# Kernel optimization log

Hardware: AMD Instinct MI355X
Metric: run time of the kernel (lower is better)

## Reference

```python
import jax, jax.numpy as jnp
import numpy as np

N = 50_000      # num_nodes
E = 1_600_000   # num_edges
R = 8           # num_relations
D = 128         # hidden_dim
L = 3           # num_layers
EPS = 1e-5


def setup_inputs() -> dict:
    key = jax.random.key(0)
    ks = jax.random.split(key, 10)
    x = jnp.arange(N, dtype=jnp.int64) if jax.config.jax_enable_x64 else jnp.arange(N, dtype=jnp.int32)
    edge_index = jax.random.randint(ks[0], (2, E), 0, N)
    edge_type = jax.random.randint(ks[1], (E,), 0, R)
    emb = jax.random.normal(ks[2], (N, D), dtype=jnp.float32) * (1.0 / np.sqrt(D))
    w_rel = jax.random.normal(ks[3], (L, R, D, D), dtype=jnp.float32) * (1.0 / np.sqrt(D))
    w_root = jax.random.normal(ks[4], (L, D, D), dtype=jnp.float32) * (1.0 / np.sqrt(D))
    bias = jax.random.normal(ks[5], (L, D), dtype=jnp.float32) * 0.01
    gamma = 1.0 + 0.1 * jax.random.normal(ks[6], (L, D), dtype=jnp.float32)
    beta = 0.1 * jax.random.normal(ks[7], (L, D), dtype=jnp.float32)
    return {"x": x, "edge_index": edge_index, "edge_type": edge_type,
            "emb": emb, "w_rel": w_rel, "w_root": w_root, "bias": bias,
            "gamma": gamma, "beta": beta}


def _layer_norm(h, g, b):
    mu = jnp.mean(h, axis=-1, keepdims=True)
    var = jnp.mean(jnp.square(h - mu), axis=-1, keepdims=True)
    return (h - mu) * jax.lax.rsqrt(var + EPS) * g + b


def _rgcn_conv(h, src, dst, etype, w_rel, w_root, b):
    # PyG RGCNConv: per-relation mean aggregation of transformed neighbors + root transform + bias
    hr = jnp.einsum('nd,rdf->rnf', h, w_rel)          # [R, N, D] relation-transformed features
    msg = hr[etype, src]                               # [E, D] gather per edge
    seg = etype * N + dst                              # combined (relation, target) segment id
    sums = jax.ops.segment_sum(msg, seg, num_segments=R * N)            # [R*N, D]
    cnt = jax.ops.segment_sum(jnp.ones((msg.shape[0],), h.dtype), seg, num_segments=R * N)
    mean = sums / jnp.maximum(cnt, 1.0)[:, None]
    agg = mean.reshape(R, N, D).sum(axis=0)            # sum over relations
    return agg + h @ w_root + b


def reference(x, edge_index, edge_type, emb, w_rel, w_root, bias, gamma, beta):
    src, dst = edge_index[0], edge_index[1]
    h = emb[x]                                         # node embedding lookup
    for i in range(L):
        h_new = _rgcn_conv(h, src, dst, edge_type, w_rel[i], w_root[i], bias[i])
        h_new = jax.nn.relu(_layer_norm(h_new, gamma[i], beta[i]))
        # dropout is identity in eval/reference mode
        h = h + h_new if i > 0 else h_new
    return h
```

## Files before the change

kernel.cpp:

```cpp
#include <hip/hip_runtime.h>

#define NN 50000
#define NE 1600000
#define NR 8
#define ND 128
#define NL 3
#define RN (NR * NN)
#define LN_EPS 1e-5f
#define PADF 132

#define NBKT 196
#define BSH 11
#define STRIDE_PB 10240
#define BIN_BLOCKS 500
#define EPB 3200
#define I4PB 800
#define MM_BLOCKS ((NN + 63) / 64)

#define PREP_G (NN * 64)
#define PREP_W (27 * 16384)
#define PREP_TOT (PREP_G + PREP_W)
#define PREP_BLOCKS ((PREP_TOT + 255) / 256)

#define WS_H    0
#define WS_ROW  14400000
#define WS_BCUR 16000064
#define WS_ADJ  16004096
#define WS_WB   22404096
#define WS_BIG  23288832
#define WS_NEED_NEW (23288832ULL + 9ULL * NN * 256)

typedef __attribute__((ext_vector_type(8))) short short8;
typedef __attribute__((ext_vector_type(4))) float float4v;
typedef __attribute__((ext_vector_type(4))) unsigned uint4v;

__device__ __forceinline__ float bflo(unsigned u) { return __uint_as_float(u << 16); }
__device__ __forceinline__ float bfhi(unsigned u) { return __uint_as_float(u & 0xFFFF0000u); }
__device__ __forceinline__ unsigned f2bf(float f) {
    unsigned u = __float_as_uint(f);
    return (u + 0x7FFFu + ((u >> 16) & 1u)) >> 16;
}
__device__ __forceinline__ unsigned pack2(float lo, float hi) {
    return f2bf(lo) | (f2bf(hi) << 16);
}

__global__ __launch_bounds__(256) void k_prepbin(const int* __restrict__ x,
                                                 const float* __restrict__ emb,
                                                 const float* __restrict__ w_rel,
                                                 const float* __restrict__ w_root,
                                                 const int* __restrict__ src,
                                                 const int* __restrict__ dst,
                                                 const int* __restrict__ et,
                                                 unsigned* __restrict__ h,
                                                 unsigned short* __restrict__ wb,
                                                 int* __restrict__ bcur,
                                                 unsigned* __restrict__ stage) {
    __shared__ int lcnt[256];
    __shared__ int loff[256];
    __shared__ int lcur[256];
    __shared__ int sbase[256];
    __shared__ int tmp[256];
    __shared__ unsigned srt[EPB];
    __shared__ unsigned char bkt[EPB];

    int tid = threadIdx.x;
    if (blockIdx.x >= BIN_BLOCKS) {
        int i = (blockIdx.x - BIN_BLOCKS) * 256 + tid;
        if (i < PREP_G) {
            int n = i >> 6, dw = i & 63;
            float2 v = *(const float2*)&emb[(size_t)x[n] * ND + 2 * dw];
            h[i] = pack2(v.x, v.y);
            return;
        }
        i -= PREP_G;
        if (i < PREP_W) {
            int m = i >> 14;
            int idx = i & 16383;
            int j = idx & 7;
            int lane = (idx >> 3) & 63;
            int ft = (idx >> 9) & 7;
            int kk = idx >> 12;
            int row = kk * 32 + (lane >> 4) * 8 + j;
            int col = ft * 16 + (lane & 15);
            const float* W = (m < 24) ? (w_rel + (size_t)m * 16384)
                                      : (w_root + (size_t)(m - 24) * 16384);
            wb[i] = (unsigned short)f2bf(W[row * ND + col]);
        }
        return;
    }

    lcnt[tid] = 0;
    __syncthreads();

    int base4 = blockIdx.x * I4PB;
    const int4* s4p = (const int4*)src;
    const int4* d4p = (const int4*)dst;
    const int4* t4p = (const int4*)et;

    for (int i4 = tid; i4 < I4PB; i4 += 256) {
        int4 d4 = d4p[base4 + i4];
        int4 t4 = t4p[base4 + i4];
        atomicAdd(&lcnt[(t4.x * NN + d4.x) >> BSH], 1);
        atomicAdd(&lcnt[(t4.y * NN + d4.y) >> BSH], 1);
        atomicAdd(&lcnt[(t4.z * NN + d4.z) >> BSH], 1);
        atomicAdd(&lcnt[(t4.w * NN + d4.w) >> BSH], 1);
    }
    __syncthreads();
    int own = lcnt[tid];
    tmp[tid] = own;
    __syncthreads();
    for (int off = 1; off < 256; off <<= 1) {
        int v = (tid >= off) ? tmp[tid - off] : 0;
        __syncthreads();
        tmp[tid] += v;
        __syncthreads();
    }
    int excl = tmp[tid] - own;
    loff[tid] = excl;
    lcur[tid] = excl;
    if (tid < NBKT) sbase[tid] = atomicAdd(&bcur[tid], own);
    __syncthreads();

    for (int i4 = tid; i4 < I4PB; i4 += 256) {
        int4 s4 = s4p[base4 + i4];
        int4 d4 = d4p[base4 + i4];
        int4 t4 = t4p[base4 + i4];
        int segs[4] = {t4.x * NN + d4.x, t4.y * NN + d4.y,
                       t4.z * NN + d4.z, t4.w * NN + d4.w};
        int srcs[4] = {s4.x, s4.y, s4.z, s4.w};
#pragma unroll
        for (int j = 0; j < 4; j++) {
            int seg = segs[j];
            int b = seg >> BSH;
            unsigned rec = ((unsigned)(seg & 2047) << 16) | (unsigned)srcs[j];
            int pos = atomicAdd(&lcur[b], 1);
            srt[pos] = rec;
            bkt[pos] = (unsigned char)b;
        }
    }
    __syncthreads();
    for (int i = tid; i < EPB; i += 256) {
        int b = bkt[i];
        int idx = sbase[b] + (i - loff[b]);
        if (idx < STRIDE_PB)
            stage[(size_t)b * STRIDE_PB + idx] = srt[i];
    }
}

__device__ __forceinline__ void binB_body(const unsigned* __restrict__ stage,
                                          const int* __restrict__ bcur,
                                          int* __restrict__ rowstart,
                                          int* __restrict__ adj,
                                          int b, int tid,
                                          int* tmp, int* lcnt2, int* loff2,
                                          unsigned short* srt2, int* misc) {
    int bv = (tid < NBKT) ? bcur[tid] : 0;
    tmp[tid] = bv;
    __syncthreads();
    for (int off = 1; off < 256; off <<= 1) {
        int v = (tid >= off) ? tmp[tid - off] : 0;
        __syncthreads();
        tmp[tid] += v;
        __syncthreads();
    }
    if (tid == b) { misc[0] = tmp[tid] - bv; misc[1] = bv; }
    for (int j = tid; j < 2048; j += 256) lcnt2[j] = 0;
    __syncthreads();

    int n = misc[1];
    n = n < STRIDE_PB ? n : STRIDE_PB;
    const unsigned* sp = stage + (size_t)b * STRIDE_PB;
    for (int i = tid; i < n; i += 256)
        atomicAdd(&lcnt2[sp[i] >> 16], 1);
    __syncthreads();

    int v8[8];
    int s8 = 0;
    int base8 = tid * 8;
#pragma unroll
    for (int j = 0; j < 8; j++) { v8[j] = lcnt2[base8 + j]; s8 += v8[j]; }
    tmp[tid] = s8;
    __syncthreads();
    for (int off = 1; off < 256; off <<= 1) {
        int v = (tid >= off) ? tmp[tid - off] : 0;
        __syncthreads();
        tmp[tid] += v;
        __syncthreads();
    }
    int run = tmp[tid] - s8;
#pragma unroll
    for (int j = 0; j < 8; j++) { loff2[base8 + j] = run; run += v8[j]; }
    __syncthreads();
    for (int j = tid; j < 2048; j += 256) lcnt2[j] = loff2[j];
    __syncthreads();

    for (int i = tid; i < n; i += 256) {
        unsigned rec = sp[i];
        int pos = atomicAdd(&lcnt2[rec >> 16], 1);
        srt2[pos] = (unsigned short)(rec & 0xFFFFu);
    }
    __syncthreads();

    int gb = misc[0];
    for (int i = tid; i < n; i += 256) adj[gb + i] = (int)srt2[i];
    int segbase = b << BSH;
    for (int j = tid; j < 2048; j += 256) {
        int seg = segbase + j;
        if (seg < RN) rowstart[seg] = gb + loff2[j];
    }
    if (b == NBKT - 1 && tid == 0) rowstart[RN] = NE;
}

typedef unsigned TRarr[16][66];

__device__ __forceinline__ void mm_body(const unsigned* __restrict__ h32,
                                        const unsigned short* __restrict__ wrel,
                                        const unsigned short* __restrict__ wroot,
                                        unsigned* __restrict__ hr,
                                        int mb, int tid,
                                        uint4* SB4, TRarr* TRp) {
    const unsigned short* SBs = (const unsigned short*)SB4;
    int wave = tid >> 6, lane = tid & 63;
    int quad = lane >> 4, l15 = lane & 15;
    int w0w = mb * 64 + wave * 16;
    int gi = w0w + l15; gi = gi < NN ? gi : NN - 1;
    int pr = l15 & 1;

    const unsigned* Hrow = h32 + (size_t)gi * 64;
    short8 afr[4];
#pragma unroll
    for (int kk = 0; kk < 4; kk++)
        afr[kk] = *(const short8*)&Hrow[kk * 16 + quad * 4];

    for (int m = 0; m < 9; m++) {
        const unsigned short* W = (m < 8) ? (wrel + (size_t)m * 16384) : wroot;
        __syncthreads();
        {
            const uint4* Wg = (const uint4*)W;
#pragma unroll
            for (int i = 0; i < 8; i++) SB4[tid + 256 * i] = Wg[tid + 256 * i];
        }
        __syncthreads();

        float4v acc[8];
#pragma unroll
        for (int i = 0; i < 8; i++) acc[i] = (float4v){0.f, 0.f, 0.f, 0.f};
#pragma unroll
        for (int kk = 0; kk < 4; kk++) {
#pragma unroll
            for (int ft = 0; ft < 8; ft++) {
                short8 bf = *(const short8*)&SBs[((kk * 8 + ft) * 64 + lane) * 8];
                acc[ft] = __builtin_amdgcn_mfma_f32_16x16x32_bf16(afr[kk], bf, acc[ft], 0, 0, 0);
            }
        }

#pragma unroll
        for (int ft = 0; ft < 8; ft++) {
            float4v part;
#pragma unroll
            for (int rg = 0; rg < 4; rg++) part[rg] = __shfl_xor(acc[ft][rg], 1, 64);
            if ((ft & 1) == pr) {
                int a = l15 >> 1;
#pragma unroll
                for (int rg = 0; rg < 4; rg++) {
                    float lo = pr ? part[rg] : acc[ft][rg];
                    float hi = pr ? acc[ft][rg] : part[rg];
                    TRp[wave][quad * 4 + rg][ft * 8 + a] = pack2(lo, hi);
                }
            }
        }
        unsigned* hrm = hr + (size_t)m * NN * 64;
#pragma unroll
        for (int ps = 0; ps < 4; ps++) {
            int ri = ps * 4 + quad;
            uint4 v = *(const uint4*)&TRp[wave][ri][l15 * 4];
            int row = w0w + ri;
            if (row < NN)
                *(uint4*)&hrm[(size_t)row * 64 + l15 * 4] = v;
        }
    }
}

__global__ __launch_bounds__(256) void k_binB_mm(const unsigned* __restrict__ stage,
                                                 const int* __restrict__ bcur,
                                                 int* __restrict__ rowstart,
                                                 int* __restrict__ adj,
                                                 const unsigned* __restrict__ h32,
                                                 const unsigned short* __restrict__ wrel,
                                                 const unsigned short* __restrict__ wroot,
                                                 unsigned* __restrict__ hr) {
    __shared__ uint4 SMEM[3104];
    int tid = threadIdx.x;
    if (blockIdx.x < NBKT) {
        int* tmp = (int*)SMEM;
        int* lcnt2 = (int*)SMEM + 256;
        int* loff2 = (int*)SMEM + 2304;
        unsigned short* srt2 = (unsigned short*)((int*)SMEM + 4352);
        int* misc = (int*)SMEM + 9472;
        binB_body(stage, bcur, rowstart, adj, blockIdx.x, tid,
                  tmp, lcnt2, loff2, srt2, misc);
    } else {
        mm_body(h32, wrel, wroot, hr, blockIdx.x - NBKT, tid,
                SMEM, (TRarr*)(SMEM + 2048));
    }
}

__global__ __launch_bounds__(256) void k_binB(const unsigned* __restrict__ stage,
                                              const int* __restrict__ bcur,
                                              int* __restrict__ rowstart,
                                              int* __restrict__ adj) {
    __shared__ uint4 SMEM[2369];
    int tid = threadIdx.x;
    int* tmp = (int*)SMEM;
    int* lcnt2 = (int*)SMEM + 256;
    int* loff2 = (int*)SMEM + 2304;
    unsigned short* srt2 = (unsigned short*)((int*)SMEM + 4352);
    int* misc = (int*)SMEM + 9472;
    binB_body(stage, bcur, rowstart, adj, blockIdx.x, tid,
              tmp, lcnt2, loff2, srt2, misc);
}

__global__ __launch_bounds__(256) void k_mm(const unsigned* __restrict__ h32,
                                            const unsigned short* __restrict__ wrel,
                                            const unsigned short* __restrict__ wroot,
                                            unsigned* __restrict__ hr) {
    __shared__ uint4 SMEM[3104];
    mm_body(h32, wrel, wroot, hr, blockIdx.x, threadIdx.x,
            SMEM, (TRarr*)(SMEM + 2048));
}

#define AGA(u)                                  \
    a0 += bflo(u.x); a1 += bfhi(u.x);           \
    a2 += bflo(u.y); a3 += bfhi(u.y);           \
    a4 += bflo(u.z); a5 += bfhi(u.z);           \
    a6 += bflo(u.w); a7 += bfhi(u.w);
#define AGC(u)                                  \
    c0 += bflo(u.x); c1 += bfhi(u.x);           \
    c2 += bflo(u.y); c3 += bfhi(u.y);           \
    c4 += bflo(u.z); c5 += bfhi(u.z);           \
    c6 += bflo(u.w); c7 += bfhi(u.w);

__global__ __launch_bounds__(256) void k_aggln(const unsigned* __restrict__ hr,
                                               unsigned* __restrict__ h32,
                                               const int* __restrict__ adj,
                                               const int* __restrict__ rowstart,
                                               const float* __restrict__ bias,
                                               const float* __restrict__ gamma,
                                               const float* __restrict__ beta,
                                               float* __restrict__ out_f,
                                               int add_res, int last) {
    int n = (blockIdx.x * 256 + threadIdx.x) >> 4;
    int l15 = threadIdx.x & 15;

    float t0 = 0.f, t1 = 0.f, t2 = 0.f, t3 = 0.f,
          t4 = 0.f, t5 = 0.f, t6 = 0.f, t7 = 0.f;

    for (int r = 0; r < NR; r++) {
        int seg = r * NN + n;
        int st = rowstart[seg], en = rowstart[seg + 1];
        st = st < 0 ? 0 : st;
        en = en > NE ? NE : en;
        const unsigned* T = hr + (size_t)r * NN * 64;

        float a0 = 0.f, a1 = 0.f, a2 = 0.f, a3 = 0.f,
              a4 = 0.f, a5 = 0.f, a6 = 0.f, a7 = 0.f;
        float c0 = 0.f, c1 = 0.f, c2 = 0.f, c3 = 0.f,
              c4 = 0.f, c5 = 0.f, c6 = 0.f, c7 = 0.f;
        int p = st;
        for (; p + 3 < en; p += 4) {
            unsigned s0 = (unsigned)adj[p],     s1 = (unsigned)adj[p + 1];
            unsigned s2 = (unsigned)adj[p + 2], s3 = (unsigned)adj[p + 3];
            uint4 u0 = *(const uint4*)&T[(size_t)s0 * 64 + l15 * 4];
            uint4 u1 = *(const uint4*)&T[(size_t)s1 * 64 + l15 * 4];
            uint4 u2 = *(const uint4*)&T[(size_t)s2 * 64 + l15 * 4];
            uint4 u3 = *(const uint4*)&T[(size_t)s3 * 64 + l15 * 4];
            AGA(u0) AGC(u1) AGA(u2) AGC(u3)
        }
        for (; p + 1 < en; p += 2) {
            unsigned s0 = (unsigned)adj[p], s1 = (unsigned)adj[p + 1];
            uint4 u0 = *(const uint4*)&T[(size_t)s0 * 64 + l15 * 4];
            uint4 u1 = *(const uint4*)&T[(size_t)s1 * 64 + l15 * 4];
            AGA(u0) AGC(u1)
        }
        if (p < en) {
            unsigned s0 = (unsigned)adj[p];
            uint4 u0 = *(const uint4*)&T[(size_t)s0 * 64 + l15 * 4];
            AGA(u0)
        }
        int d = en - st;
        float sc = 1.0f / (float)(d > 1 ? d : 1);
        t0 += (a0 + c0) * sc; t1 += (a1 + c1) * sc;
        t2 += (a2 + c2) * sc; t3 += (a3 + c3) * sc;
        t4 += (a4 + c4) * sc; t5 += (a5 + c5) * sc;
        t6 += (a6 + c6) * sc; t7 += (a7 + c7) * sc;
    }

    {
        uint4 u = *(const uint4*)&hr[((size_t)8 * NN + n) * 64 + l15 * 4];
        t0 += bflo(u.x); t1 += bfhi(u.x);
        t2 += bflo(u.y); t3 += bfhi(u.y);
        t4 += bflo(u.z); t5 += bfhi(u.z);
        t6 += bflo(u.w); t7 += bfhi(u.w);
    }
    int f0 = 8 * l15;
    {
        float4 b0 = *(const float4*)&bias[f0];
        float4 b1 = *(const float4*)&bias[f0 + 4];
        t0 += b0.x; t1 += b0.y; t2 += b0.z; t3 += b0.w;
        t4 += b1.x; t5 += b1.y; t6 += b1.z; t7 += b1.w;
    }

    float s = t0 + t1 + t2 + t3 + t4 + t5 + t6 + t7;
#pragma unroll
    for (int off = 1; off < 16; off <<= 1) s += __shfl_xor(s, off, 64);
    float mu = s * (1.0f / ND);
    float e0 = t0 - mu, e1 = t1 - mu, e2 = t2 - mu, e3 = t3 - mu,
          e4 = t4 - mu, e5 = t5 - mu, e6 = t6 - mu, e7 = t7 - mu;
    float vs = e0 * e0 + e1 * e1 + e2 * e2 + e3 * e3 +
               e4 * e4 + e5 * e5 + e6 * e6 + e7 * e7;
#pragma unroll
    for (int off = 1; off < 16; off <<= 1) vs += __shfl_xor(vs, off, 64);
    float rr = rsqrtf(vs * (1.0f / ND) + LN_EPS);

    float4 g0 = *(const float4*)&gamma[f0];
    float4 g1 = *(const float4*)&gamma[f0 + 4];
    float4 be0 = *(const float4*)&beta[f0];
    float4 be1 = *(const float4*)&beta[f0 + 4];
    float o0 = fmaxf(e0 * rr * g0.x + be0.x, 0.0f);
    float o1 = fmaxf(e1 * rr * g0.y + be0.y, 0.0f);
    float o2 = fmaxf(e2 * rr * g0.z + be0.z, 0.0f);
    float o3 = fmaxf(e3 * rr * g0.w + be0.w, 0.0f);
    float o4 = fmaxf(e4 * rr * g1.x + be1.x, 0.0f);
    float o5 = fmaxf(e5 * rr * g1.y + be1.y, 0.0f);
    float o6 = fmaxf(e6 * rr * g1.z + be1.z, 0.0f);
    float o7 = fmaxf(e7 * rr * g1.w + be1.w, 0.0f);

    if (add_res) {
        uint4 u = *(const uint4*)&h32[(size_t)n * 64 + l15 * 4];
        o0 += bflo(u.x); o1 += bfhi(u.x);
        o2 += bflo(u.y); o3 += bfhi(u.y);
        o4 += bflo(u.z); o5 += bfhi(u.z);
        o6 += bflo(u.w); o7 += bfhi(u.w);
    }
    if (last) {
        *(float4*)&out_f[(size_t)n * ND + f0] = make_float4(o0, o1, o2, o3);
        *(float4*)&out_f[(size_t)n * ND + f0 + 4] = make_float4(o4, o5, o6, o7);
    } else {
        uint4 w;
        w.x = pack2(o0, o1); w.y = pack2(o2, o3);
        w.z = pack2(o4, o5); w.w = pack2(o6, o7);
        *(uint4*)&h32[(size_t)n * 64 + l15 * 4] = w;
    }
}


__global__ __launch_bounds__(256) void k_agg(const unsigned* __restrict__ h32,
                                             const int* __restrict__ adj,
                                             const int* __restrict__ rowstart,
                                             unsigned* __restrict__ S) {
    int q = (blockIdx.x * 256 + threadIdx.x) >> 4;
    int l15 = threadIdx.x & 15;
    int r = q / NN;
    int n = q - r * NN;
    int st = rowstart[q], en = rowstart[q + 1];
    st = st < 0 ? 0 : st;
    en = en > NE ? NE : en;
    float a0 = 0.f, a1 = 0.f, a2 = 0.f, a3 = 0.f,
          a4 = 0.f, a5 = 0.f, a6 = 0.f, a7 = 0.f;
    float c0 = 0.f, c1 = 0.f, c2 = 0.f, c3 = 0.f,
          c4 = 0.f, c5 = 0.f, c6 = 0.f, c7 = 0.f;
    int p = st;
    for (; p + 3 < en; p += 4) {
        unsigned s0 = (unsigned)adj[p],     s1 = (unsigned)adj[p + 1];
        unsigned s2 = (unsigned)adj[p + 2], s3 = (unsigned)adj[p + 3];
        uint4 u0 = *(const uint4*)&h32[(size_t)s0 * 64 + l15 * 4];
        uint4 u1 = *(const uint4*)&h32[(size_t)s1 * 64 + l15 * 4];
        uint4 u2 = *(const uint4*)&h32[(size_t)s2 * 64 + l15 * 4];
        uint4 u3 = *(const uint4*)&h32[(size_t)s3 * 64 + l15 * 4];
        AGA(u0) AGC(u1) AGA(u2) AGC(u3)
    }
    for (; p < en; p++) {
        unsigned s0 = (unsigned)adj[p];
        uint4 u0 = *(const uint4*)&h32[(size_t)s0 * 64 + l15 * 4];
        AGA(u0)
    }
    int d = en - st;
    float sc = 1.0f / (float)(d > 1 ? d : 1);
    a0 = (a0 + c0) * sc; a1 = (a1 + c1) * sc;
    a2 = (a2 + c2) * sc; a3 = (a3 + c3) * sc;
    a4 = (a4 + c4) * sc; a5 = (a5 + c5) * sc;
    a6 = (a6 + c6) * sc; a7 = (a7 + c7) * sc;
    uint4v w;
    w.x = pack2(a0, a1); w.y = pack2(a2, a3);
    w.z = pack2(a4, a5); w.w = pack2(a6, a7);
    __builtin_nontemporal_store(w, (uint4v*)&S[(size_t)n * 512 + r * 64 + l15 * 4]);
}

__global__ __launch_bounds__(256) void k_gemm(const unsigned* __restrict__ S,
                                              unsigned* __restrict__ h32,
                                              const unsigned short* __restrict__ wrel,
                                              const unsigned short* __restrict__ wroot,
                                              const float* __restrict__ bias,
                                              const float* __restrict__ gamma,
                                              const float* __restrict__ beta,
                                              float* __restrict__ out_f,
                                              int add_res, int last) {
    __shared__ char smraw[4 * 16 * PADF * 4];
    float* SLF = (float*)smraw;
    uint4* SB4 = (uint4*)smraw;
    const unsigned short* SBs = (const unsigned short*)smraw;

    int tid = threadIdx.x;
    int wave = tid >> 6, lane = tid & 63;
    int quad = lane >> 4, l15 = lane & 15;
    int w0 = blockIdx.x * 64 + wave * 16;
    int gi = w0 + l15; gi = gi < NN ? gi : NN - 1;
    float* WF = SLF + wave * 16 * PADF;

    float4v acc[8];
#pragma unroll
    for (int i = 0; i < 8; i++) acc[i] = (float4v){0.f, 0.f, 0.f, 0.f};

    const unsigned* Sr = S + (size_t)gi * 512;
    for (int r = 0; r < NR; r++) {
        short8 afr[4];
#pragma unroll
        for (int kk = 0; kk < 4; kk++)
            afr[kk] = *(const short8*)&Sr[r * 64 + kk * 16 + quad * 4];
        __syncthreads();
        {
            const uint4* Wg = (const uint4*)(wrel + (size_t)r * 16384);
#pragma unroll
            for (int i = 0; i < 8; i++) SB4[tid + 256 * i] = Wg[tid + 256 * i];
        }
        __syncthreads();
#pragma unroll
        for (int kk = 0; kk < 4; kk++) {
#pragma unroll
            for (int ft = 0; ft < 8; ft++) {
                short8 bf = *(const short8*)&SBs[((kk * 8 + ft) * 64 + lane) * 8];
                acc[ft] = __builtin_amdgcn_mfma_f32_16x16x32_bf16(afr[kk], bf, acc[ft], 0, 0, 0);
            }
        }
    }
    {
        const unsigned* Hr = h32 + (size_t)gi * 64;
        short8 afr[4];
#pragma unroll
        for (int kk = 0; kk < 4; kk++)
            afr[kk] = *(const short8*)&Hr[kk * 16 + quad * 4];
        __syncthreads();
        {
            const uint4* Wg = (const uint4*)wroot;
#pragma unroll
            for (int i = 0; i < 8; i++) SB4[tid + 256 * i] = Wg[tid + 256 * i];
        }
        __syncthreads();
#pragma unroll
        for (int kk = 0; kk < 4; kk++) {
#pragma unroll
            for (int ft = 0; ft < 8; ft++) {
                short8 bf = *(const short8*)&SBs[((kk * 8 + ft) * 64 + lane) * 8];
                acc[ft] = __builtin_amdgcn_mfma_f32_16x16x32_bf16(afr[kk], bf, acc[ft], 0, 0, 0);
            }
        }
    }
    __syncthreads();

#pragma unroll
    for (int ft = 0; ft < 8; ft++)
#pragma unroll
        for (int rg = 0; rg < 4; rg++)
            WF[(quad * 4 + rg) * PADF + ft * 16 + l15] = acc[ft][rg];

    float2 bia = *(const float2*)&bias[2 * lane];
    float2 gam = *(const float2*)&gamma[2 * lane];
    float2 bet = *(const float2*)&beta[2 * lane];

    for (int i = 0; i < 16; i++) {
        int g = w0 + i;
        if (g >= NN) continue;
        float v0 = WF[i * PADF + 2 * lane] + bia.x;
        float v1 = WF[i * PADF + 2 * lane + 1] + bia.y;
        float s = v0 + v1;
#pragma unroll
        for (int off = 32; off > 0; off >>= 1) s += __shfl_xor(s, off, 64);
        float mu = s * (1.0f / ND);
        float e0 = v0 - mu, e1 = v1 - mu;
        float vs = e0 * e0 + e1 * e1;
#pragma unroll
        for (int off = 32; off > 0; off >>= 1) vs += __shfl_xor(vs, off, 64);
        float rr = rsqrtf(vs * (1.0f / ND) + LN_EPS);
        float o0 = fmaxf(e0 * rr * gam.x + bet.x, 0.0f);
        float o1 = fmaxf(e1 * rr * gam.y + bet.y, 0.0f);
        if (add_res) {
            unsigned u = h32[(size_t)g * 64 + lane];
            o0 += bflo(u);
            o1 += bfhi(u);
        }
        if (last) {
            *(float2*)&out_f[(size_t)g * ND + 2 * lane] = make_float2(o0, o1);
        } else {
            h32[(size_t)g * 64 + lane] = pack2(o0, o1);
        }
    }
}

extern "C" void kernel_launch(void* const* d_in, const int* in_sizes, int n_in,
                              void* d_out, int out_size, void* d_ws, size_t ws_size,
                              hipStream_t stream) {
    const int*   x      = (const int*)d_in[0];
    const int*   ei     = (const int*)d_in[1];
    const int*   et     = (const int*)d_in[2];
    const float* emb    = (const float*)d_in[3];
    const float* w_rel  = (const float*)d_in[4];
    const float* w_root = (const float*)d_in[5];
    const float* bias   = (const float*)d_in[6];
    const float* gamma  = (const float*)d_in[7];
    const float* beta   = (const float*)d_in[8];
    float* out = (float*)d_out;

    char* ws = (char*)d_ws;
    unsigned* h        = (unsigned*)(ws + WS_H);
    int*      rowstart = (int*)     (ws + WS_ROW);
    int*      bcur     = (int*)     (ws + WS_BCUR);
    int*      adj      = (int*)     (ws + WS_ADJ);
    unsigned short* wb = (unsigned short*)(ws + WS_WB);
    unsigned* big      = (unsigned*)(ws + WS_BIG);
    unsigned* stage    = (unsigned*)d_out;

    const int* src = ei;
    const int* dst = ei + NE;

    hipMemsetAsync(bcur, 0, NBKT * sizeof(int), stream);

    k_prepbin<<<BIN_BLOCKS + PREP_BLOCKS, 256, 0, stream>>>(
        x, emb, w_rel, w_root, src, dst, et, h, wb, bcur, stage);

    if (ws_size >= WS_NEED_NEW) {
        k_binB_mm<<<NBKT + MM_BLOCKS, 256, 0, stream>>>(
            stage, bcur, rowstart, adj,
            h, wb, wb + (size_t)24 * 16384, big);
        k_aggln<<<NN * 16 / 256, 256, 0, stream>>>(
            big, h, adj, rowstart,
            bias, gamma, beta, out, 0, 0);
        for (int l = 1; l < NL; l++) {
            k_mm<<<MM_BLOCKS, 256, 0, stream>>>(
                h, wb + (size_t)l * 8 * 16384, wb + (size_t)(24 + l) * 16384, big);
            k_aggln<<<NN * 16 / 256, 256, 0, stream>>>(
                big, h, adj, rowstart,
                bias + l * ND, gamma + l * ND, beta + l * ND,
                out, 1, l == NL - 1);
        }
    } else {
        k_binB<<<NBKT, 256, 0, stream>>>(stage, bcur, rowstart, adj);
        for (int l = 0; l < NL; l++) {
            k_agg<<<RN * 16 / 256, 256, 0, stream>>>(h, adj, rowstart, big);
            k_gemm<<<(NN + 63) / 64, 256, 0, stream>>>(
                big, h,
                wb + (size_t)l * 8 * 16384, wb + (size_t)(24 + l) * 16384,
                bias + l * ND, gamma + l * ND, beta + l * ND,
                out, l > 0, l == NL - 1);
        }
    }
}
```

Measured before the change: 502.6 us.

## Use one wave per node in aggregation, two row groups per matmul block

The aggregation+LayerNorm kernel now maps a full 64-lane wave to each node, with each lane loading one 32-bit bf16 pair per neighbour row. It previously used 16 lanes per node with 128-bit loads. This is meant to spread each node's gather across more threads and use wave-wide reductions, at the cost of more, narrower memory requests. The standalone matmul kernel is templated so each block processes two 64-row groups, reusing each shared-memory weight tile across twice as many rows. Binning blocks are doubled with half the edges per block.

```diff
diff --git a/kernel.cpp b/kernel.cpp
--- a/kernel.cpp
+++ b/kernel.cpp
@@ -12,10 +12,11 @@
 #define NBKT 196
 #define BSH 11
 #define STRIDE_PB 10240
-#define BIN_BLOCKS 500
-#define EPB 3200
-#define I4PB 800
-#define MM_BLOCKS ((NN + 63) / 64)
+#define BIN_BLOCKS 1000
+#define EPB 1600
+#define I4PB 400
+#define MM_BLOCKS_SA ((NN + 127) / 128)
+#define MM_BLOCKS_FU ((NN + 63) / 64)
 
 #define PREP_G (NN * 64)
 #define PREP_W (27 * 16384)
@@ -213,6 +214,7 @@
 
 typedef unsigned TRarr[16][66];
 
+template <int NG>
 __device__ __forceinline__ void mm_body(const unsigned* __restrict__ h32,
                                         const unsigned short* __restrict__ wrel,
                                         const unsigned short* __restrict__ wroot,
@@ -222,15 +224,19 @@
     const unsigned short* SBs = (const unsigned short*)SB4;
     int wave = tid >> 6, lane = tid & 63;
     int quad = lane >> 4, l15 = lane & 15;
-    int w0w = mb * 64 + wave * 16;
-    int gi = w0w + l15; gi = gi < NN ? gi : NN - 1;
     int pr = l15 & 1;
 
-    const unsigned* Hrow = h32 + (size_t)gi * 64;
-    short8 afr[4];
-#pragma unroll
-    for (int kk = 0; kk < 4; kk++)
-        afr[kk] = *(const short8*)&Hrow[kk * 16 + quad * 4];
+    int rbase[NG];
+    short8 af[NG][4];
+#pragma unroll
+    for (int g = 0; g < NG; g++) {
+        rbase[g] = mb * (64 * NG) + g * 64 + wave * 16;
+        int gi = rbase[g] + l15; gi = gi < NN ? gi : NN - 1;
+        const unsigned* H = h32 + (size_t)gi * 64;
+#pragma unroll
+        for (int kk = 0; kk < 4; kk++)
+            af[g][kk] = *(const short8*)&H[kk * 16 + quad * 4];
+    }
 
     for (int m = 0; m < 9; m++) {
         const unsigned short* W = (m < 8) ? (wrel + (size_t)m * 16384) : wroot;
@@ -242,41 +248,48 @@
         }
         __syncthreads();
 
-        float4v acc[8];
-#pragma unroll
-        for (int i = 0; i < 8; i++) acc[i] = (float4v){0.f, 0.f, 0.f, 0.f};
+        float4v ac[NG][8];
+#pragma unroll
+        for (int g = 0; g < NG; g++)
+#pragma unroll
+            for (int i = 0; i < 8; i++) ac[g][i] = (float4v){0.f, 0.f, 0.f, 0.f};
 #pragma unroll
         for (int kk = 0; kk < 4; kk++) {
 #pragma unroll
             for (int ft = 0; ft < 8; ft++) {
                 short8 bf = *(const short8*)&SBs[((kk * 8 + ft) * 64 + lane) * 8];
-                acc[ft] = __builtin_amdgcn_mfma_f32_16x16x32_bf16(afr[kk], bf, acc[ft], 0, 0, 0);
+#pragma unroll
+                for (int g = 0; g < NG; g++)
+                    ac[g][ft] = __builtin_amdgcn_mfma_f32_16x16x32_bf16(af[g][kk], bf, ac[g][ft], 0, 0, 0);
             }
         }
 
-#pragma unroll
-        for (int ft = 0; ft < 8; ft++) {
-            float4v part;
-#pragma unroll
-            for (int rg = 0; rg < 4; rg++) part[rg] = __shfl_xor(acc[ft][rg], 1, 64);
-            if ((ft & 1) == pr) {
-                int a = l15 >> 1;
-#pragma unroll
-                for (int rg = 0; rg < 4; rg++) {
-                    float lo = pr ? part[rg] : acc[ft][rg];
-                    float hi = pr ? acc[ft][rg] : part[rg];
-                    TRp[wave][quad * 4 + rg][ft * 8 + a] = pack2(lo, hi);
+        unsigned* hrm = hr + (size_t)m * NN * 64;
+#pragma unroll
+        for (int g = 0; g < NG; g++) {
+#pragma unroll
+            for (int ft = 0; ft < 8; ft++) {
+                float4v part;
+#pragma unroll
+                for (int rg = 0; rg < 4; rg++) part[rg] = __shfl_xor(ac[g][ft][rg], 1, 64);
+                if ((ft & 1) == pr) {
+                    int a = l15 >> 1;
+#pragma unroll
+                    for (int rg = 0; rg < 4; rg++) {
+                        float lo = pr ? part[rg] : ac[g][ft][rg];
+                        float hi = pr ? ac[g][ft][rg] : part[rg];
+                        TRp[wave][quad * 4 + rg][ft * 8 + a] = pack2(lo, hi);
+                    }
                 }
             }
-        }
-        unsigned* hrm = hr + (size_t)m * NN * 64;
-#pragma unroll
-        for (int ps = 0; ps < 4; ps++) {
-            int ri = ps * 4 + quad;
-            uint4 v = *(const uint4*)&TRp[wave][ri][l15 * 4];
-            int row = w0w + ri;
-            if (row < NN)
-                *(uint4*)&hrm[(size_t)row * 64 + l15 * 4] = v;
+#pragma unroll
+            for (int ps = 0; ps < 4; ps++) {
+                int ri = ps * 4 + quad;
+                uint4 v = *(const uint4*)&TRp[wave][ri][l15 * 4];
+                int row = rbase[g] + ri;
+                if (row < NN)
+                    *(uint4*)&hrm[(size_t)row * 64 + l15 * 4] = v;
+            }
         }
     }
 }
@@ -300,8 +313,8 @@
         binB_body(stage, bcur, rowstart, adj, blockIdx.x, tid,
                   tmp, lcnt2, loff2, srt2, misc);
     } else {
-        mm_body(h32, wrel, wroot, hr, blockIdx.x - NBKT, tid,
-                SMEM, (TRarr*)(SMEM + 2048));
+        mm_body<1>(h32, wrel, wroot, hr, blockIdx.x - NBKT, tid,
+                   SMEM, (TRarr*)(SMEM + 2048));
     }
 }
 
@@ -325,9 +338,95 @@
                                             const unsigned short* __restrict__ wroot,
                                             unsigned* __restrict__ hr) {
     __shared__ uint4 SMEM[3104];
-    mm_body(h32, wrel, wroot, hr, blockIdx.x, threadIdx.x,
-            SMEM, (TRarr*)(SMEM + 2048));
-}
+    mm_body<2>(h32, wrel, wroot, hr, blockIdx.x, threadIdx.x,
+               SMEM, (TRarr*)(SMEM + 2048));
+}
+
+__global__ __launch_bounds__(256) void k_aggln(const unsigned* __restrict__ hr,
+                                               unsigned* __restrict__ h32,
+                                               const int* __restrict__ adj,
+                                               const int* __restrict__ rowstart,
+                                               const float* __restrict__ bias,
+                                               const float* __restrict__ gamma,
+                                               const float* __restrict__ beta,
+                                               float* __restrict__ out_f,
+                                               int add_res, int last) {
+    int wave = threadIdx.x >> 6;
+    int lane = threadIdx.x & 63;
+    int n = blockIdx.x * 4 + wave;
+
+    float t0 = 0.f, t1 = 0.f;
+    for (int r = 0; r < NR; r++) {
+        int seg = r * NN + n;
+        int st = rowstart[seg], en = rowstart[seg + 1];
+        st = st < 0 ? 0 : st;
+        en = en > NE ? NE : en;
+        const unsigned* T = hr + (size_t)r * NN * 64 + lane;
+
+        float a0 = 0.f, a1 = 0.f, b0 = 0.f, b1 = 0.f;
+        int p = st;
+        for (; p + 3 < en; p += 4) {
+            unsigned s0 = (unsigned)adj[p],     s1 = (unsigned)adj[p + 1];
+            unsigned s2 = (unsigned)adj[p + 2], s3 = (unsigned)adj[p + 3];
+            unsigned u0 = T[(size_t)s0 * 64];
+            unsigned u1 = T[(size_t)s1 * 64];
+            unsigned u2 = T[(size_t)s2 * 64];
+            unsigned u3 = T[(size_t)s3 * 64];
+            a0 += bflo(u0); a1 += bfhi(u0);
+            b0 += bflo(u1); b1 += bfhi(u1);
+            a0 += bflo(u2); a1 += bfhi(u2);
+            b0 += bflo(u3); b1 += bfhi(u3);
+        }
+        for (; p + 1 < en; p += 2) {
+            unsigned s0 = (unsigned)adj[p], s1 = (unsigned)adj[p + 1];
+            unsigned u0 = T[(size_t)s0 * 64];
+            unsigned u1 = T[(size_t)s1 * 64];
+            a0 += bflo(u0); a1 += bfhi(u0);
+            b0 += bflo(u1); b1 += bfhi(u1);
+        }
+        if (p < en) {
+            unsigned u0 = T[(size_t)(unsigned)adj[p] * 64];
+            a0 += bflo(u0); a1 += bfhi(u0);
+        }
+        int d = en - st;
+        float sc = 1.0f / (float)(d > 1 ? d : 1);
+        t0 += (a0 + b0) * sc;
+        t1 += (a1 + b1) * sc;
+    }
+
+    {
+        unsigned u = hr[((size_t)8 * NN + n) * 64 + lane];
+        t0 += bflo(u); t1 += bfhi(u);
+    }
+    float2 bia = *(const float2*)&bias[2 * lane];
+    t0 += bia.x; t1 += bia.y;
+
+    float s = t0 + t1;
+#pragma unroll
+    for (int off = 32; off > 0; off >>= 1) s += __shfl_xor(s, off, 64);
+    float mu = s * (1.0f / ND);
+    float e0 = t0 - mu, e1 = t1 - mu;
+    float vs = e0 * e0 + e1 * e1;
+#pragma unroll
+    for (int off = 32; off > 0; off >>= 1) vs += __shfl_xor(vs, off, 64);
+    float rr = rsqrtf(vs * (1.0f / ND) + LN_EPS);
+
+    float2 gam = *(const float2*)&gamma[2 * lane];
+    float2 bet = *(const float2*)&beta[2 * lane];
+    float o0 = fmaxf(e0 * rr * gam.x + bet.x, 0.0f);
+    float o1 = fmaxf(e1 * rr * gam.y + bet.y, 0.0f);
+
+    if (add_res) {
+        unsigned u = h32[(size_t)n * 64 + lane];
+        o0 += bflo(u); o1 += bfhi(u);
+    }
+    if (last) {
+        *(float2*)&out_f[(size_t)n * ND + 2 * lane] = make_float2(o0, o1);
+    } else {
+        h32[(size_t)n * 64 + lane] = pack2(o0, o1);
+    }
+}
+
 
 #define AGA(u)                                  \
     a0 += bflo(u.x); a1 += bfhi(u.x);           \
@@ -339,120 +438,6 @@
     c2 += bflo(u.y); c3 += bfhi(u.y);           \
     c4 += bflo(u.z); c5 += bfhi(u.z);           \
     c6 += bflo(u.w); c7 += bfhi(u.w);
-
-__global__ __launch_bounds__(256) void k_aggln(const unsigned* __restrict__ hr,
-                                               unsigned* __restrict__ h32,
-                                               const int* __restrict__ adj,
-                                               const int* __restrict__ rowstart,
-                                               const float* __restrict__ bias,
-                                               const float* __restrict__ gamma,
-                                               const float* __restrict__ beta,
-                                               float* __restrict__ out_f,
-                                               int add_res, int last) {
-    int n = (blockIdx.x * 256 + threadIdx.x) >> 4;
-    int l15 = threadIdx.x & 15;
-
-    float t0 = 0.f, t1 = 0.f, t2 = 0.f, t3 = 0.f,
-          t4 = 0.f, t5 = 0.f, t6 = 0.f, t7 = 0.f;
-
-    for (int r = 0; r < NR; r++) {
-        int seg = r * NN + n;
-        int st = rowstart[seg], en = rowstart[seg + 1];
-        st = st < 0 ? 0 : st;
-        en = en > NE ? NE : en;
-        const unsigned* T = hr + (size_t)r * NN * 64;
-
-        float a0 = 0.f, a1 = 0.f, a2 = 0.f, a3 = 0.f,
-              a4 = 0.f, a5 = 0.f, a6 = 0.f, a7 = 0.f;
-        float c0 = 0.f, c1 = 0.f, c2 = 0.f, c3 = 0.f,
-              c4 = 0.f, c5 = 0.f, c6 = 0.f, c7 = 0.f;
-        int p = st;
-        for (; p + 3 < en; p += 4) {
-            unsigned s0 = (unsigned)adj[p],     s1 = (unsigned)adj[p + 1];
-            unsigned s2 = (unsigned)adj[p + 2], s3 = (unsigned)adj[p + 3];
-            uint4 u0 = *(const uint4*)&T[(size_t)s0 * 64 + l15 * 4];
-            uint4 u1 = *(const uint4*)&T[(size_t)s1 * 64 + l15 * 4];
-            uint4 u2 = *(const uint4*)&T[(size_t)s2 * 64 + l15 * 4];
-            uint4 u3 = *(const uint4*)&T[(size_t)s3 * 64 + l15 * 4];
-            AGA(u0) AGC(u1) AGA(u2) AGC(u3)
-        }
-        for (; p + 1 < en; p += 2) {
-            unsigned s0 = (unsigned)adj[p], s1 = (unsigned)adj[p + 1];
-            uint4 u0 = *(const uint4*)&T[(size_t)s0 * 64 + l15 * 4];
-            uint4 u1 = *(const uint4*)&T[(size_t)s1 * 64 + l15 * 4];
-            AGA(u0) AGC(u1)
-        }
-        if (p < en) {
-            unsigned s0 = (unsigned)adj[p];
-            uint4 u0 = *(const uint4*)&T[(size_t)s0 * 64 + l15 * 4];
-            AGA(u0)
-        }
-        int d = en - st;
-        float sc = 1.0f / (float)(d > 1 ? d : 1);
-        t0 += (a0 + c0) * sc; t1 += (a1 + c1) * sc;
-        t2 += (a2 + c2) * sc; t3 += (a3 + c3) * sc;
-        t4 += (a4 + c4) * sc; t5 += (a5 + c5) * sc;
-        t6 += (a6 + c6) * sc; t7 += (a7 + c7) * sc;
-    }
-
-    {
-        uint4 u = *(const uint4*)&hr[((size_t)8 * NN + n) * 64 + l15 * 4];
-        t0 += bflo(u.x); t1 += bfhi(u.x);
-        t2 += bflo(u.y); t3 += bfhi(u.y);
-        t4 += bflo(u.z); t5 += bfhi(u.z);
-        t6 += bflo(u.w); t7 += bfhi(u.w);
-    }
-    int f0 = 8 * l15;
-    {
-        float4 b0 = *(const float4*)&bias[f0];
-        float4 b1 = *(const float4*)&bias[f0 + 4];
-        t0 += b0.x; t1 += b0.y; t2 += b0.z; t3 += b0.w;
-        t4 += b1.x; t5 += b1.y; t6 += b1.z; t7 += b1.w;
-    }
-
-    float s = t0 + t1 + t2 + t3 + t4 + t5 + t6 + t7;
-#pragma unroll
-    for (int off = 1; off < 16; off <<= 1) s += __shfl_xor(s, off, 64);
-    float mu = s * (1.0f / ND);
-    float e0 = t0 - mu, e1 = t1 - mu, e2 = t2 - mu, e3 = t3 - mu,
-          e4 = t4 - mu, e5 = t5 - mu, e6 = t6 - mu, e7 = t7 - mu;
-    float vs = e0 * e0 + e1 * e1 + e2 * e2 + e3 * e3 +
-               e4 * e4 + e5 * e5 + e6 * e6 + e7 * e7;
-#pragma unroll
-    for (int off = 1; off < 16; off <<= 1) vs += __shfl_xor(vs, off, 64);
-    float rr = rsqrtf(vs * (1.0f / ND) + LN_EPS);
-
-    float4 g0 = *(const float4*)&gamma[f0];
-    float4 g1 = *(const float4*)&gamma[f0 + 4];
-    float4 be0 = *(const float4*)&beta[f0];
-    float4 be1 = *(const float4*)&beta[f0 + 4];
-    float o0 = fmaxf(e0 * rr * g0.x + be0.x, 0.0f);
-    float o1 = fmaxf(e1 * rr * g0.y + be0.y, 0.0f);
-    float o2 = fmaxf(e2 * rr * g0.z + be0.z, 0.0f);
-    float o3 = fmaxf(e3 * rr * g0.w + be0.w, 0.0f);
-    float o4 = fmaxf(e4 * rr * g1.x + be1.x, 0.0f);
-    float o5 = fmaxf(e5 * rr * g1.y + be1.y, 0.0f);
-    float o6 = fmaxf(e6 * rr * g1.z + be1.z, 0.0f);
-    float o7 = fmaxf(e7 * rr * g1.w + be1.w, 0.0f);
-
-    if (add_res) {
-        uint4 u = *(const uint4*)&h32[(size_t)n * 64 + l15 * 4];
-        o0 += bflo(u.x); o1 += bfhi(u.x);
-        o2 += bflo(u.y); o3 += bfhi(u.y);
-        o4 += bflo(u.z); o5 += bfhi(u.z);
-        o6 += bflo(u.w); o7 += bfhi(u.w);
-    }
-    if (last) {
-        *(float4*)&out_f[(size_t)n * ND + f0] = make_float4(o0, o1, o2, o3);
-        *(float4*)&out_f[(size_t)n * ND + f0 + 4] = make_float4(o4, o5, o6, o7);
-    } else {
-        uint4 w;
-        w.x = pack2(o0, o1); w.y = pack2(o2, o3);
-        w.z = pack2(o4, o5); w.w = pack2(o6, o7);
-        *(uint4*)&h32[(size_t)n * 64 + l15 * 4] = w;
-    }
-}
-
 
 __global__ __launch_bounds__(256) void k_agg(const unsigned* __restrict__ h32,
                                              const int* __restrict__ adj,
@@ -638,16 +623,16 @@
         x, emb, w_rel, w_root, src, dst, et, h, wb, bcur, stage);
 
     if (ws_size >= WS_NEED_NEW) {
-        k_binB_mm<<<NBKT + MM_BLOCKS, 256, 0, stream>>>(
+        k_binB_mm<<<NBKT + MM_BLOCKS_FU, 256, 0, stream>>>(
             stage, bcur, rowstart, adj,
             h, wb, wb + (size_t)24 * 16384, big);
-        k_aggln<<<NN * 16 / 256, 256, 0, stream>>>(
+        k_aggln<<<NN / 4, 256, 0, stream>>>(
             big, h, adj, rowstart,
             bias, gamma, beta, out, 0, 0);
         for (int l = 1; l < NL; l++) {
-            k_mm<<<MM_BLOCKS, 256, 0, stream>>>(
+            k_mm<<<MM_BLOCKS_SA, 256, 0, stream>>>(
                 h, wb + (size_t)l * 8 * 16384, wb + (size_t)(24 + l) * 16384, big);
-            k_aggln<<<NN * 16 / 256, 256, 0, stream>>>(
+            k_aggln<<<NN / 4, 256, 0, stream>>>(
                 big, h, adj, rowstart,
                 bias + l * ND, gamma + l * ND, beta + l * ND,
                 out, 1, l == NL - 1);
```

Result: slower. 598.3 us (+19.0%).
